# Kernel tuning notes

Measured on AMD Instinct MI355X. Metric: run time of the kernel, lower is better.

The kernel has to match this reference:

```python
import jax, jax.numpy as jnp
import numpy as np

B, N, C, H = 4, 1024, 1024, 16
HD = C // H
SCALE = HD ** -0.5


def setup_inputs() -> dict:
    key = jax.random.key(0)
    ks = jax.random.split(key, 6)
    s = 0.02
    return {
        "x": jax.random.normal(ks[0], (B, N, C), jnp.float32),
        "k_in": jax.random.normal(ks[1], (B, N, C), jnp.float32),
        "attn_add": jax.random.uniform(ks[2], (B, N, N), jnp.float32),
        "Wq": jax.random.normal(ks[3], (C, C), jnp.float32) * s,
        "Wkv": jax.random.normal(ks[4], (C, 2 * C), jnp.float32) * s,
        "Wproj": jax.random.normal(ks[5], (C, C), jnp.float32) * s,
        "bproj": jnp.zeros((C,), jnp.float32),
    }


def reference(x, k_in, attn_add, Wq, Wkv, Wproj, bproj):
    b, nx, c = x.shape
    nk = k_in.shape[1]
    # q: [B, H, N_x, HD]
    q = (x @ Wq).reshape(b, nx, H, HD).transpose(0, 2, 1, 3)
    # kv: [B, N_k, 2, H, HD] -> k, v each [B, H, N_k, HD]
    kv = (k_in @ Wkv).reshape(b, nk, 2, H, HD)
    k = kv[:, :, 0].transpose(0, 2, 1, 3)
    v = kv[:, :, 1].transpose(0, 2, 1, 3)
    # scores: [B, H, N_x, N_k]
    attn = jnp.einsum("bhnd,bhmd->bhnm", q, k) * SCALE
    attn = jax.nn.softmax(attn, axis=-1)
    # mask-modulated re-softmax: attn_add [B, N_x, N_k] broadcast over heads
    attn = attn * attn_add[:, None, :, :]
    attn = jax.nn.softmax(attn, axis=-1)
    out = jnp.einsum("bhnm,bhmd->bhnd", attn, v)
    out = out.transpose(0, 2, 1, 3).reshape(b, nx, c)
    return out @ Wproj + bproj
```

## Files before the change

### kernel.cpp

```cpp
#include <hip/hip_runtime.h>
#include <cmath>


#define Bb 4
#define Nn 1024
#define Cc 1024
#define Hh 16
#define HD 64

typedef unsigned short u16;
typedef short bf16x8 __attribute__((ext_vector_type(8)));
typedef float f32x4 __attribute__((ext_vector_type(4)));
typedef unsigned short u16x4 __attribute__((ext_vector_type(4)));
typedef unsigned short u16x8 __attribute__((ext_vector_type(8)));
typedef __attribute__((address_space(1))) const void* gptr_t;
typedef __attribute__((address_space(3))) void* lptr_t;

__device__ __forceinline__ u16 f2b(float f) {
  union { float f; unsigned u; } x; x.f = f;
  unsigned u = x.u;
  return (u16)((u + 0x7FFFu + ((u >> 16) & 1u)) >> 16);
}
__device__ __forceinline__ float b2f(u16 h) {
  union { unsigned u; float f; } x; x.u = ((unsigned)h) << 16;
  return x.f;
}

__global__ __launch_bounds__(256) void prep_big(
    const float* __restrict__ x, const float* __restrict__ kin,
    const float* __restrict__ af,
    u16* __restrict__ xh, u16* __restrict__ kinh, u16* __restrict__ ab) {
  const int i = (blockIdx.x * 256 + threadIdx.x) * 8;
  f32x4 x0 = *(const f32x4*)(x + i),   x1 = *(const f32x4*)(x + i + 4);
  f32x4 k0 = *(const f32x4*)(kin + i), k1 = *(const f32x4*)(kin + i + 4);
  f32x4 a0 = *(const f32x4*)(af + i),  a1 = *(const f32x4*)(af + i + 4);
  u16x8 xo, ko, ao;
  #pragma unroll
  for (int j = 0; j < 4; ++j) {
    xo[j] = f2b(x0[j]); xo[j + 4] = f2b(x1[j]);
    ko[j] = f2b(k0[j]); ko[j + 4] = f2b(k1[j]);
    ao[j] = f2b(a0[j]); ao[j + 4] = f2b(a1[j]);
  }
  *(u16x8*)(xh + i) = xo;
  *(u16x8*)(kinh + i) = ko;
  *(u16x8*)(ab + i) = ao;
}

__global__ __launch_bounds__(256) void prep_wt(
    const float* __restrict__ Wq, const float* __restrict__ Wkv,
    const float* __restrict__ Wp,
    u16* __restrict__ WqT, u16* __restrict__ WkvTh, u16* __restrict__ WpTh) {
  __shared__ float tile[64][65];
  int id = blockIdx.x;
  const float* src; int srcld; u16* dh; int ot0, it0;
  if (id < 256)      { src = Wq;  srcld = 1024; dh = WqT;
                       ot0 = (id >> 4) * 64; it0 = (id & 15) * 64; }
  else if (id < 768) { id -= 256; src = Wkv; srcld = 2048; dh = WkvTh;
                       ot0 = (id >> 4) * 64; it0 = (id & 15) * 64; }
  else               { id -= 768; src = Wp;  srcld = 1024; dh = WpTh;
                       ot0 = (id >> 4) * 64; it0 = (id & 15) * 64; }
  const int tr = threadIdx.x >> 4;
  const int tc = (threadIdx.x & 15) * 4;
  #pragma unroll
  for (int rr = 0; rr < 4; ++rr) {
    const int r = rr * 16 + tr;
    f32x4 v = *(const f32x4*)&src[(size_t)(it0 + r) * srcld + ot0 + tc];
    tile[r][tc] = v[0]; tile[r][tc + 1] = v[1];
    tile[r][tc + 2] = v[2]; tile[r][tc + 3] = v[3];
  }
  __syncthreads();
  #pragma unroll
  for (int rr = 0; rr < 4; ++rr) {
    const int o = rr * 16 + tr;
    u16x4 hv;
    #pragma unroll
    for (int j = 0; j < 4; ++j) hv[j] = f2b(tile[tc + j][o]);
    *(u16x4*)(dh + (size_t)(ot0 + o) * 1024 + it0 + tc) = hv;
  }
}

__global__ __launch_bounds__(256) void gemm_qkv(
    const u16* __restrict__ xh, const u16* __restrict__ kinh,
    const u16* __restrict__ WqT, const u16* __restrict__ WkvTh,
    u16* __restrict__ qb, u16* __restrict__ kb, u16* __restrict__ vtb,
    float* __restrict__ vtf) {
  constexpr int K = 1024;
  __shared__ u16 As[64 * 32];
  __shared__ u16 Bs[128 * 32];
  const int tid = threadIdx.x;
  const int wave = tid >> 6, lane = tid & 63;
  const int l15 = lane & 15, l4 = lane >> 4;
  const int y = blockIdx.y;
  const bool isq = (y < 8);
  const u16* A  = isq ? xh : kinh;
  const u16* Bt = isq ? WqT : WkvTh;
  const int m0 = blockIdx.x * 64;
  const int n0 = (isq ? y : (y - 8)) * 128;
  const int wr = wave >> 1, wc = wave & 1;
  const int srow = tid >> 2, scol = (tid & 3) * 8;
  f32x4 acc[2][4] = {};
  const u16* gA  = A  + (size_t)(m0 + srow) * K + scol;
  const u16* gB0 = Bt + (size_t)(n0 + srow) * K + scol;
  const u16* gB1 = Bt + (size_t)(n0 + 64 + srow) * K + scol;
  for (int kt = 0; kt < K; kt += 32) {
    __syncthreads();
    __builtin_amdgcn_global_load_lds((gptr_t)(gA  + kt), (lptr_t)(As + wave * 512), 16, 0, 0);
    __builtin_amdgcn_global_load_lds((gptr_t)(gB0 + kt), (lptr_t)(Bs + wave * 512), 16, 0, 0);
    __builtin_amdgcn_global_load_lds((gptr_t)(gB1 + kt), (lptr_t)(Bs + 2048 + wave * 512), 16, 0, 0);
    __syncthreads();
    bf16x8 af[2], bf_[4];
    #pragma unroll
    for (int i = 0; i < 2; ++i)
      af[i] = *(const bf16x8*)(As + (wr * 32 + i * 16 + l15) * 32 + l4 * 8);
    #pragma unroll
    for (int i = 0; i < 4; ++i)
      bf_[i] = *(const bf16x8*)(Bs + (wc * 64 + i * 16 + l15) * 32 + l4 * 8);
    #pragma unroll
    for (int mi = 0; mi < 2; ++mi)
      #pragma unroll
      for (int ni = 0; ni < 4; ++ni)
        acc[mi][ni] = __builtin_amdgcn_mfma_f32_16x16x32_bf16(af[mi], bf_[ni], acc[mi][ni], 0, 0, 0);
  }
  #pragma unroll
  for (int mi = 0; mi < 2; ++mi)
    #pragma unroll
    for (int ni = 0; ni < 4; ++ni)
      #pragma unroll
      for (int r = 0; r < 4; ++r) {
        const int grow = m0 + wr * 32 + mi * 16 + l4 * 4 + r;
        const int gcol = n0 + wc * 64 + ni * 16 + l15;
        const int bb = grow >> 10, n = grow & 1023;
        const float v = acc[mi][ni][r];
        if (isq) {
          const int hh = gcol >> 6, d = gcol & 63;
          qb[(((size_t)(bb * Hh + hh)) * Nn + n) * HD + d] = f2b(v);
        } else if (gcol < 1024) {
          const int hh = gcol >> 6, d = gcol & 63;
          kb[(((size_t)(bb * Hh + hh)) * Nn + n) * HD + d] = f2b(v);
        } else {
          const int cv = gcol - 1024;
          const int hh = cv >> 6, d = cv & 63;
          const size_t o = (((size_t)(bb * Hh + hh)) * HD + d) * Nn + n;
          vtf[o] = v;
          vtb[o] = f2b(v);
        }
      }
}

__global__ __launch_bounds__(256) void sumv_kernel(const float* __restrict__ vtf,
                                                   float* __restrict__ sv) {
  const int bh = blockIdx.x >> 2, d16 = blockIdx.x & 3;
  const int t = threadIdx.x;
  const int d = d16 * 16 + (t >> 4), part = t & 15;
  const float* src = vtf + ((size_t)bh * HD + d) * Nn + part * 64;
  float s = 0.f;
  #pragma unroll
  for (int i = 0; i < 64; i += 4) {
    f32x4 v = *(const f32x4*)(src + i);
    s += v[0] + v[1] + v[2] + v[3];
  }
  s += __shfl_xor(s, 1, 64);
  s += __shfl_xor(s, 2, 64);
  s += __shfl_xor(s, 4, 64);
  s += __shfl_xor(s, 8, 64);
  if (part == 0) sv[(size_t)bh * HD + d] = s;
}

__global__ __launch_bounds__(256, 3) void attn_kernel(
    const u16* __restrict__ qb, const u16* __restrict__ kb,
    const u16* __restrict__ vtb, const float* __restrict__ sv,
    const u16* __restrict__ ab, u16* __restrict__ aoh) {
  __shared__ u16 pt[32 * 128];
  __shared__ u16 at[32 * 136];
  __shared__ float Lp_lds[4][32];
  __shared__ float Ep_lds[4][32];
  __shared__ float Lred[32];
  __shared__ float Ered[32];

  const int tid = threadIdx.x;
  const int wave = tid >> 6, lane = tid & 63;
  const int l15 = lane & 15, l4 = lane >> 4;
  const int bid = (blockIdx.x & 7) * 256 + (blockIdx.x >> 3);
  const int qt = bid & 31, h = (bid >> 5) & 15, b = bid >> 9;
  const size_t bh = (size_t)(b * Hh + h);
  const u16* qg = qb + (bh * Nn + qt * 32) * HD;
  const u16* kg = kb + bh * Nn * HD;
  const u16* vg = vtb + bh * HD * Nn;
  constexpr float C1 = 0.125f * 1.44269504f;

  bf16x8 qf[2][2];
  #pragma unroll
  for (int t2 = 0; t2 < 2; ++t2)
    #pragma unroll
    for (int ks = 0; ks < 2; ++ks)
      qf[t2][ks] = *(const bf16x8*)(qg + (t2 * 16 + l15) * HD + ks * 32 + l4 * 8);

  const int arow = tid >> 3;
  const int acol = (tid & 7) * 16;
  const u16* agp = ab + ((size_t)(b * Nn + qt * 32 + arow)) * Nn + acol;

  {
    bf16x8 a0 = *(const bf16x8*)agp;
    bf16x8 a1 = *(const bf16x8*)(agp + 8);
    *(bf16x8*)(at + arow * 136 + acol) = a0;
    *(bf16x8*)(at + arow * 136 + acol + 8) = a1;
  }
  const u16* kbase = kg + (size_t)(wave * 32 + l15) * HD + l4 * 8;
  bf16x8 kcur0 = *(const bf16x8*)kbase;
  bf16x8 kcur1 = *(const bf16x8*)(kbase + 32);
  bf16x8 kcur2 = *(const bf16x8*)(kbase + 16 * HD);
  bf16x8 kcur3 = *(const bf16x8*)(kbase + 16 * HD + 32);
  __syncthreads();

  float Lp[2][4] = {};
  float ep[2][4] = {};
  f32x4 oacc[2] = {};

  for (int mt = 0; mt < 8; ++mt) {
    bf16x8 kn0, kn1, kn2, kn3;
    bf16x8 an0, an1;
    if (mt < 7) {
      const u16* kr = kbase + (size_t)(mt + 1) * 128 * HD;
      kn0 = *(const bf16x8*)kr;
      kn1 = *(const bf16x8*)(kr + 32);
      kn2 = *(const bf16x8*)(kr + 16 * HD);
      kn3 = *(const bf16x8*)(kr + 16 * HD + 32);
      an0 = *(const bf16x8*)(agp + (mt + 1) * 128);
      an1 = *(const bf16x8*)(agp + (mt + 1) * 128 + 8);
    }
    bf16x8 vf[4];
    #pragma unroll
    for (int k2 = 0; k2 < 4; ++k2)
      vf[k2] = *(const bf16x8*)(vg + (size_t)(wave * 16 + l15) * Nn + (mt << 7) + k2 * 32 + l4 * 8);

    #pragma unroll
    for (int cf = 0; cf < 2; ++cf) {
      bf16x8 ka  = cf ? kcur2 : kcur0;
      bf16x8 kbv = cf ? kcur3 : kcur1;
      f32x4 s0 = {}, s1 = {};
      s0 = __builtin_amdgcn_mfma_f32_16x16x32_bf16(qf[0][0], ka,  s0, 0, 0, 0);
      s0 = __builtin_amdgcn_mfma_f32_16x16x32_bf16(qf[0][1], kbv, s0, 0, 0, 0);
      s1 = __builtin_amdgcn_mfma_f32_16x16x32_bf16(qf[1][0], ka,  s1, 0, 0, 0);
      s1 = __builtin_amdgcn_mfma_f32_16x16x32_bf16(qf[1][1], kbv, s1, 0, 0, 0);
      const int mloc = wave * 32 + cf * 16 + l15;
      #pragma unroll
      for (int r = 0; r < 4; ++r) {
        const int q0 = l4 * 4 + r;
        const float c0 = __builtin_amdgcn_exp2f(s0[r] * C1);
        const float c1 = __builtin_amdgcn_exp2f(s1[r] * C1);
        Lp[0][r] += c0;
        Lp[1][r] += c1;
        const float a0 = b2f(at[q0 * 136 + mloc]);
        const float a1 = b2f(at[(q0 + 16) * 136 + mloc]);
        const float p0 = c0 * a0;
        const float p1 = c1 * a1;
        ep[0][r] += p0;
        ep[1][r] += p1;
        unsigned dpk;
        asm("v_cvt_pk_bf16_f32 %0, %1, %2" : "=v"(dpk) : "v"(p0), "v"(p1));
        const int col = mloc ^ ((q0 & 7) << 3);
        pt[q0 * 128 + col] = (u16)dpk;
        pt[(q0 + 16) * 128 + col] = (u16)(dpk >> 16);
      }
    }
    kcur0 = kn0; kcur1 = kn1; kcur2 = kn2; kcur3 = kn3;
    __syncthreads();

    if (mt < 7) {
      *(bf16x8*)(at + arow * 136 + acol) = an0;
      *(bf16x8*)(at + arow * 136 + acol + 8) = an1;
    }
    #pragma unroll
    for (int t2 = 0; t2 < 2; ++t2)
      #pragma unroll
      for (int k2 = 0; k2 < 4; ++k2) {
        const int row = t2 * 16 + l15;
        bf16x8 df = *(const bf16x8*)(pt + row * 128 + ((k2 * 32 + l4 * 8) ^ ((row & 7) << 3)));
        oacc[t2] = __builtin_amdgcn_mfma_f32_16x16x32_bf16(df, vf[k2], oacc[t2], 0, 0, 0);
      }
    __syncthreads();
  }

  #pragma unroll
  for (int t2 = 0; t2 < 2; ++t2)
    #pragma unroll
    for (int r = 0; r < 4; ++r) {
      float lv = Lp[t2][r];
      lv += __shfl_xor(lv, 1, 64); lv += __shfl_xor(lv, 2, 64);
      lv += __shfl_xor(lv, 4, 64); lv += __shfl_xor(lv, 8, 64);
      float ev = ep[t2][r];
      ev += __shfl_xor(ev, 1, 64); ev += __shfl_xor(ev, 2, 64);
      ev += __shfl_xor(ev, 4, 64); ev += __shfl_xor(ev, 8, 64);
      if (l15 == 0) {
        Lp_lds[wave][t2 * 16 + l4 * 4 + r] = lv;
        Ep_lds[wave][t2 * 16 + l4 * 4 + r] = ev;
      }
    }
  __syncthreads();
  if (tid < 32) {
    Lred[tid] = 1.0f / (Lp_lds[0][tid] + Lp_lds[1][tid] + Lp_lds[2][tid] + Lp_lds[3][tid]);
    Ered[tid] = Ep_lds[0][tid] + Ep_lds[1][tid] + Ep_lds[2][tid] + Ep_lds[3][tid];
  }
  __syncthreads();

  {
    const int d = wave * 16 + l15;
    const float svd = sv[bh * HD + d];
    #pragma unroll
    for (int t2 = 0; t2 < 2; ++t2)
      #pragma unroll
      for (int r = 0; r < 4; ++r) {
        const int row = t2 * 16 + l4 * 4 + r;
        const float linv = Lred[row];
        const float E = fmaf(linv, Ered[row], 1024.0f);
        const float ov = fmaf(linv, oacc[t2][r], svd) / E;
        const int n = qt * 32 + row;
        aoh[((size_t)b * Nn + n) * Cc + h * HD + d] = f2b(ov);
      }
  }
}

__global__ __launch_bounds__(256) void gemm_proj(
    const u16* __restrict__ Ah, const u16* __restrict__ Bh,
    const float* __restrict__ bias, float* __restrict__ dstf) {
  constexpr int K = 1024;
  __shared__ u16 As[64 * 32];
  __shared__ u16 Bs[128 * 32];
  const int tid = threadIdx.x;
  const int wave = tid >> 6, lane = tid & 63;
  const int l15 = lane & 15, l4 = lane >> 4;
  const int m0 = blockIdx.x * 64, n0 = blockIdx.y * 128;
  const int wr = wave >> 1, wc = wave & 1;
  const int srow = tid >> 2, scol = (tid & 3) * 8;
  f32x4 acc[2][4] = {};
  const u16* gA  = Ah + (size_t)(m0 + srow) * K + scol;
  const u16* gB0 = Bh + (size_t)(n0 + srow) * K + scol;
  const u16* gB1 = Bh + (size_t)(n0 + 64 + srow) * K + scol;
  for (int kt = 0; kt < K; kt += 32) {
    __syncthreads();
    __builtin_amdgcn_global_load_lds((gptr_t)(gA  + kt), (lptr_t)(As + wave * 512), 16, 0, 0);
    __builtin_amdgcn_global_load_lds((gptr_t)(gB0 + kt), (lptr_t)(Bs + wave * 512), 16, 0, 0);
    __builtin_amdgcn_global_load_lds((gptr_t)(gB1 + kt), (lptr_t)(Bs + 2048 + wave * 512), 16, 0, 0);
    __syncthreads();
    bf16x8 af[2], bf_[4];
    #pragma unroll
    for (int i = 0; i < 2; ++i)
      af[i] = *(const bf16x8*)(As + (wr * 32 + i * 16 + l15) * 32 + l4 * 8);
    #pragma unroll
    for (int i = 0; i < 4; ++i)
      bf_[i] = *(const bf16x8*)(Bs + (wc * 64 + i * 16 + l15) * 32 + l4 * 8);
    #pragma unroll
    for (int mi = 0; mi < 2; ++mi)
      #pragma unroll
      for (int ni = 0; ni < 4; ++ni)
        acc[mi][ni] = __builtin_amdgcn_mfma_f32_16x16x32_bf16(af[mi], bf_[ni], acc[mi][ni], 0, 0, 0);
  }
  #pragma unroll
  for (int mi = 0; mi < 2; ++mi)
    #pragma unroll
    for (int ni = 0; ni < 4; ++ni)
      #pragma unroll
      for (int r = 0; r < 4; ++r) {
        const int grow = m0 + wr * 32 + mi * 16 + l4 * 4 + r;
        const int gcol = n0 + wc * 64 + ni * 16 + l15;
        dstf[(size_t)grow * Cc + gcol] = acc[mi][ni][r] + bias[gcol];
      }
}

extern "C" void kernel_launch(void* const* d_in, const int* in_sizes, int n_in,
                              void* d_out, int out_size, void* d_ws, size_t ws_size,
                              hipStream_t stream) {
  (void)in_sizes; (void)n_in; (void)out_size; (void)ws_size;
  const float* x   = (const float*)d_in[0];
  const float* kin = (const float*)d_in[1];
  const float* af  = (const float*)d_in[2];
  const float* Wq  = (const float*)d_in[3];
  const float* Wkv = (const float*)d_in[4];
  const float* Wp  = (const float*)d_in[5];
  const float* bp  = (const float*)d_in[6];
  float* out = (float*)d_out;

  char* w = (char*)d_ws;
  auto take = [&](size_t bytes) { char* p = w; w += (bytes + 255) & ~(size_t)255; return p; };
  u16* WqT    = (u16*)take(2097152);
  u16* WkvTh  = (u16*)take(4194304);
  u16* WpTh   = (u16*)take(2097152);
  u16* xh     = (u16*)take(8388608);
  u16* kinh   = (u16*)take(8388608);
  u16* ab     = (u16*)take(8388608);
  u16* qb     = (u16*)take(8388608);
  u16* kb     = (u16*)take(8388608);
  u16* vtb    = (u16*)take(8388608);
  float* vtf  = (float*)take(16777216);
  float* sv   = (float*)take(16384);
  u16* aoh    = (u16*)take(8388608);

  prep_big<<<dim3(2048), dim3(256), 0, stream>>>(x, kin, af, xh, kinh, ab);
  prep_wt<<<dim3(1024), dim3(256), 0, stream>>>(Wq, Wkv, Wp, WqT, WkvTh, WpTh);

  gemm_qkv<<<dim3(64, 24), dim3(256), 0, stream>>>(xh, kinh, WqT, WkvTh, qb, kb, vtb, vtf);
  sumv_kernel<<<dim3(256), dim3(256), 0, stream>>>(vtf, sv);
  attn_kernel<<<dim3(2048), dim3(256), 0, stream>>>(qb, kb, vtb, sv, ab, aoh);
  gemm_proj<<<dim3(64, 8), dim3(256), 0, stream>>>(aoh, WpTh, bp, out);
}
```

Baseline: 176.4 us.

## Restructure attention so each wave owns a 16-query tile independently

```diff
diff --git a/kernel.cpp b/kernel.cpp
--- a/kernel.cpp
+++ b/kernel.cpp
@@ -170,153 +170,88 @@
     const u16* __restrict__ qb, const u16* __restrict__ kb,
     const u16* __restrict__ vtb, const float* __restrict__ sv,
     const u16* __restrict__ ab, u16* __restrict__ aoh) {
-  __shared__ u16 pt[32 * 128];
-  __shared__ u16 at[32 * 136];
-  __shared__ float Lp_lds[4][32];
-  __shared__ float Ep_lds[4][32];
-  __shared__ float Lred[32];
-  __shared__ float Ered[32];
+  __shared__ u16 ct[4][16 * 40];
 
   const int tid = threadIdx.x;
   const int wave = tid >> 6, lane = tid & 63;
   const int l15 = lane & 15, l4 = lane >> 4;
-  const int bid = (blockIdx.x & 7) * 256 + (blockIdx.x >> 3);
-  const int qt = bid & 31, h = (bid >> 5) & 15, b = bid >> 9;
+  const int bid = (blockIdx.x & 7) * 128 + (blockIdx.x >> 3);
+  const int unit = bid * 4 + wave;
+  const int qt = unit & 63, h = (unit >> 6) & 15, b = unit >> 10;
   const size_t bh = (size_t)(b * Hh + h);
-  const u16* qg = qb + (bh * Nn + qt * 32) * HD;
-  const u16* kg = kb + bh * Nn * HD;
-  const u16* vg = vtb + bh * HD * Nn;
+  const u16* qg = qb + (bh * Nn + qt * 16) * HD;
+  const u16* kl = kb + bh * Nn * HD + (size_t)l15 * HD + l4 * 8;
+  const u16* vl = vtb + bh * HD * Nn + (size_t)l15 * Nn + l4 * 8;
+  const u16* ag = ab + ((size_t)(b * Nn + qt * 16 + l15)) * Nn + l4 * 8;
+  u16* cw = ct[wave];
   constexpr float C1 = 0.125f * 1.44269504f;
 
-  bf16x8 qf[2][2];
-  #pragma unroll
-  for (int t2 = 0; t2 < 2; ++t2)
-    #pragma unroll
-    for (int ks = 0; ks < 2; ++ks)
-      qf[t2][ks] = *(const bf16x8*)(qg + (t2 * 16 + l15) * HD + ks * 32 + l4 * 8);
-
-  const int arow = tid >> 3;
-  const int acol = (tid & 7) * 16;
-  const u16* agp = ab + ((size_t)(b * Nn + qt * 32 + arow)) * Nn + acol;
-
-  {
-    bf16x8 a0 = *(const bf16x8*)agp;
-    bf16x8 a1 = *(const bf16x8*)(agp + 8);
-    *(bf16x8*)(at + arow * 136 + acol) = a0;
-    *(bf16x8*)(at + arow * 136 + acol + 8) = a1;
-  }
-  const u16* kbase = kg + (size_t)(wave * 32 + l15) * HD + l4 * 8;
-  bf16x8 kcur0 = *(const bf16x8*)kbase;
-  bf16x8 kcur1 = *(const bf16x8*)(kbase + 32);
-  bf16x8 kcur2 = *(const bf16x8*)(kbase + 16 * HD);
-  bf16x8 kcur3 = *(const bf16x8*)(kbase + 16 * HD + 32);
-  __syncthreads();
-
-  float Lp[2][4] = {};
-  float ep[2][4] = {};
-  f32x4 oacc[2] = {};
-
-  for (int mt = 0; mt < 8; ++mt) {
-    bf16x8 kn0, kn1, kn2, kn3;
-    bf16x8 an0, an1;
-    if (mt < 7) {
-      const u16* kr = kbase + (size_t)(mt + 1) * 128 * HD;
-      kn0 = *(const bf16x8*)kr;
-      kn1 = *(const bf16x8*)(kr + 32);
-      kn2 = *(const bf16x8*)(kr + 16 * HD);
-      kn3 = *(const bf16x8*)(kr + 16 * HD + 32);
-      an0 = *(const bf16x8*)(agp + (mt + 1) * 128);
-      an1 = *(const bf16x8*)(agp + (mt + 1) * 128 + 8);
-    }
-    bf16x8 vf[4];
-    #pragma unroll
-    for (int k2 = 0; k2 < 4; ++k2)
-      vf[k2] = *(const bf16x8*)(vg + (size_t)(wave * 16 + l15) * Nn + (mt << 7) + k2 * 32 + l4 * 8);
-
+  bf16x8 qf0 = *(const bf16x8*)(qg + l15 * HD + l4 * 8);
+  bf16x8 qf1 = *(const bf16x8*)(qg + l15 * HD + 32 + l4 * 8);
+
+  float Lp[4] = {};
+  float ep = 0.f;
+  f32x4 oacc[4] = {};
+
+  for (int mi = 0; mi < 32; ++mi) {
+    const int m0 = mi * 32;
     #pragma unroll
     for (int cf = 0; cf < 2; ++cf) {
-      bf16x8 ka  = cf ? kcur2 : kcur0;
-      bf16x8 kbv = cf ? kcur3 : kcur1;
-      f32x4 s0 = {}, s1 = {};
-      s0 = __builtin_amdgcn_mfma_f32_16x16x32_bf16(qf[0][0], ka,  s0, 0, 0, 0);
-      s0 = __builtin_amdgcn_mfma_f32_16x16x32_bf16(qf[0][1], kbv, s0, 0, 0, 0);
-      s1 = __builtin_amdgcn_mfma_f32_16x16x32_bf16(qf[1][0], ka,  s1, 0, 0, 0);
-      s1 = __builtin_amdgcn_mfma_f32_16x16x32_bf16(qf[1][1], kbv, s1, 0, 0, 0);
-      const int mloc = wave * 32 + cf * 16 + l15;
+      const u16* kr = kl + (size_t)(m0 + cf * 16) * HD;
+      bf16x8 k0 = *(const bf16x8*)kr;
+      bf16x8 k1 = *(const bf16x8*)(kr + 32);
+      f32x4 s = {};
+      s = __builtin_amdgcn_mfma_f32_16x16x32_bf16(qf0, k0, s, 0, 0, 0);
+      s = __builtin_amdgcn_mfma_f32_16x16x32_bf16(qf1, k1, s, 0, 0, 0);
       #pragma unroll
       for (int r = 0; r < 4; ++r) {
-        const int q0 = l4 * 4 + r;
-        const float c0 = __builtin_amdgcn_exp2f(s0[r] * C1);
-        const float c1 = __builtin_amdgcn_exp2f(s1[r] * C1);
-        Lp[0][r] += c0;
-        Lp[1][r] += c1;
-        const float a0 = b2f(at[q0 * 136 + mloc]);
-        const float a1 = b2f(at[(q0 + 16) * 136 + mloc]);
-        const float p0 = c0 * a0;
-        const float p1 = c1 * a1;
-        ep[0][r] += p0;
-        ep[1][r] += p1;
-        unsigned dpk;
-        asm("v_cvt_pk_bf16_f32 %0, %1, %2" : "=v"(dpk) : "v"(p0), "v"(p1));
-        const int col = mloc ^ ((q0 & 7) << 3);
-        pt[q0 * 128 + col] = (u16)dpk;
-        pt[(q0 + 16) * 128 + col] = (u16)(dpk >> 16);
+        const float c = __builtin_amdgcn_exp2f(s[r] * C1);
+        Lp[r] += c;
+        cw[(l4 * 4 + r) * 40 + cf * 16 + l15] = f2b(c);
       }
     }
-    kcur0 = kn0; kcur1 = kn1; kcur2 = kn2; kcur3 = kn3;
-    __syncthreads();
-
-    if (mt < 7) {
-      *(bf16x8*)(at + arow * 136 + acol) = an0;
-      *(bf16x8*)(at + arow * 136 + acol + 8) = an1;
+    bf16x8 c8 = *(const bf16x8*)(cw + l15 * 40 + l4 * 8);
+    bf16x8 a8 = *(const bf16x8*)(ag + m0);
+    union PF { unsigned u[4]; bf16x8 v; } pf;
+    #pragma unroll
+    for (int j = 0; j < 4; ++j) {
+      const float p0 = b2f((u16)c8[2 * j])     * b2f((u16)a8[2 * j]);
+      const float p1 = b2f((u16)c8[2 * j + 1]) * b2f((u16)a8[2 * j + 1]);
+      ep += p0 + p1;
+      asm("v_cvt_pk_bf16_f32 %0, %1, %2" : "=v"(pf.u[j]) : "v"(p0), "v"(p1));
     }
     #pragma unroll
-    for (int t2 = 0; t2 < 2; ++t2)
-      #pragma unroll
-      for (int k2 = 0; k2 < 4; ++k2) {
-        const int row = t2 * 16 + l15;
-        bf16x8 df = *(const bf16x8*)(pt + row * 128 + ((k2 * 32 + l4 * 8) ^ ((row & 7) << 3)));
-        oacc[t2] = __builtin_amdgcn_mfma_f32_16x16x32_bf16(df, vf[k2], oacc[t2], 0, 0, 0);
-      }
-    __syncthreads();
-  }
-
-  #pragma unroll
-  for (int t2 = 0; t2 < 2; ++t2)
+    for (int dt = 0; dt < 4; ++dt) {
+      bf16x8 vf = *(const bf16x8*)(vl + (size_t)(dt * 16) * Nn + m0);
+      oacc[dt] = __builtin_amdgcn_mfma_f32_16x16x32_bf16(pf.v, vf, oacc[dt], 0, 0, 0);
+    }
+  }
+
+  float linv[4];
+  #pragma unroll
+  for (int r = 0; r < 4; ++r) {
+    float v = Lp[r];
+    v += __shfl_xor(v, 1, 64); v += __shfl_xor(v, 2, 64);
+    v += __shfl_xor(v, 4, 64); v += __shfl_xor(v, 8, 64);
+    linv[r] = 1.0f / v;
+  }
+  ep += __shfl_xor(ep, 16, 64);
+  ep += __shfl_xor(ep, 32, 64);
+
+  float e1r[4];
+  #pragma unroll
+  for (int r = 0; r < 4; ++r) e1r[r] = __shfl(ep, l4 * 4 + r, 64);
+  #pragma unroll
+  for (int dt = 0; dt < 4; ++dt) {
+    const int d = dt * 16 + l15;
+    const float svd = sv[bh * HD + d];
     #pragma unroll
     for (int r = 0; r < 4; ++r) {
-      float lv = Lp[t2][r];
-      lv += __shfl_xor(lv, 1, 64); lv += __shfl_xor(lv, 2, 64);
-      lv += __shfl_xor(lv, 4, 64); lv += __shfl_xor(lv, 8, 64);
-      float ev = ep[t2][r];
-      ev += __shfl_xor(ev, 1, 64); ev += __shfl_xor(ev, 2, 64);
-      ev += __shfl_xor(ev, 4, 64); ev += __shfl_xor(ev, 8, 64);
-      if (l15 == 0) {
-        Lp_lds[wave][t2 * 16 + l4 * 4 + r] = lv;
-        Ep_lds[wave][t2 * 16 + l4 * 4 + r] = ev;
-      }
+      const int q0 = l4 * 4 + r;
+      const float E = fmaf(linv[r], e1r[r], 1024.0f);
+      const float ov = fmaf(linv[r], oacc[dt][r], svd) / E;
+      aoh[((size_t)b * Nn + qt * 16 + q0) * Cc + h * HD + d] = f2b(ov);
     }
-  __syncthreads();
-  if (tid < 32) {
-    Lred[tid] = 1.0f / (Lp_lds[0][tid] + Lp_lds[1][tid] + Lp_lds[2][tid] + Lp_lds[3][tid]);
-    Ered[tid] = Ep_lds[0][tid] + Ep_lds[1][tid] + Ep_lds[2][tid] + Ep_lds[3][tid];
-  }
-  __syncthreads();
-
-  {
-    const int d = wave * 16 + l15;
-    const float svd = sv[bh * HD + d];
-    #pragma unroll
-    for (int t2 = 0; t2 < 2; ++t2)
-      #pragma unroll
-      for (int r = 0; r < 4; ++r) {
-        const int row = t2 * 16 + l4 * 4 + r;
-        const float linv = Lred[row];
-        const float E = fmaf(linv, Ered[row], 1024.0f);
-        const float ov = fmaf(linv, oacc[t2][r], svd) / E;
-        const int n = qt * 32 + row;
-        aoh[((size_t)b * Nn + n) * Cc + h * HD + d] = f2b(ov);
-      }
   }
 }
 
@@ -400,6 +335,6 @@
 
   gemm_qkv<<<dim3(64, 24), dim3(256), 0, stream>>>(xh, kinh, WqT, WkvTh, qb, kb, vtb, vtf);
   sumv_kernel<<<dim3(256), dim3(256), 0, stream>>>(vtf, sv);
-  attn_kernel<<<dim3(2048), dim3(256), 0, stream>>>(qb, kb, vtb, sv, ab, aoh);
+  attn_kernel<<<dim3(1024), dim3(256), 0, stream>>>(qb, kb, vtb, sv, ab, aoh);
   gemm_proj<<<dim3(64, 8), dim3(256), 0, stream>>>(aoh, WpTh, bp, out);
 }
```

Result: slower. 236.3 us (+33.9%).
